# Kernel optimization log

Hardware: AMD Instinct MI355X
Metric: run time of the kernel (lower is better)

The kernel has to match this reference:

```python
import jax, jax.numpy as jnp
import numpy as np

N, C_IN, C_OUT, W, K = 4, 64, 64, 81920, 10


def setup_inputs() -> dict:
    key = jax.random.key(0)
    k1, k2, k3, k4 = jax.random.split(key, 4)
    inp = {}
    inp["input"] = jax.random.normal(k1, (N, C_IN, 1, W), dtype=jnp.float32)
    inp["conv_table"] = jax.random.randint(k2, (W, K), 0, W, dtype=jnp.int64)
    # kaiming-uniform-like init for weight, uniform for bias (values are arbitrary for a numeric baseline)
    fan_in = C_IN * K  # in_dim * 10 * 1
    wb = float(np.sqrt(6.0 / fan_in))
    inp["weight"] = jax.random.uniform(k3, (C_OUT, C_IN, K, 1), dtype=jnp.float32, minval=-wb, maxval=wb)
    bb = float(1.0 / np.sqrt(fan_in))
    inp["bias"] = jax.random.uniform(k4, (C_OUT,), dtype=jnp.float32, minval=-bb, maxval=bb)
    return inp


def reference(input, conv_table, weight, bias):
    # input: (N, C, 1, W); conv_table: (W, 10) neighbor indices into W.
    # Torch: x = input[..., conv_table.T].squeeze() -> (N, C, 10, W); conv2d with (O, C, 10, 1)
    # kernel collapses the neighbor axis: a fixed-adjacency gather + per-pixel weighted sum.
    x = input[:, :, 0, :]                  # (N, C, W)
    gathered = x[:, :, conv_table]         # (N, C, W, 10)  -- irregular gather
    out = jnp.einsum("ncwk,ock->now", gathered, weight[..., 0])  # (N, O, W)
    out = out + bias[None, :, None]
    out = jax.nn.relu(out)
    return out[:, :, None, :]              # (N, O, 1, W) to match conv2d output
```

## Files before the change

### kernel.cpp

```cpp
#include <hip/hip_runtime.h>
#include <hip/hip_bf16.h>

#define N_    4
#define W_    81920
#define K_    10
#define CIO   64

typedef unsigned short u16;
typedef __attribute__((ext_vector_type(8))) short bf16x8;
typedef __attribute__((ext_vector_type(4))) float f32x4;

static __device__ __forceinline__ u16 f2bf(float f) {
    union { float f; unsigned u; } v; v.f = f;
    unsigned r = (v.u + 0x7FFFu + ((v.u >> 16) & 1u)) >> 16;
    return (u16)r;
}

__global__ __launch_bounds__(256) void prep_weights_k(const float* __restrict__ w,
                                                      u16* __restrict__ wfrag) {
    int g = blockIdx.x * 256 + threadIdx.x;
    if (g >= 5120) return;
    int lane = g & 63;
    int f = g >> 6;
    int ot = f & 3, s = f >> 2;
    int o  = ot * 16 + (lane & 15);
    int kb = s * 32 + (lane >> 4) * 8;
    bf16x8 pack;
#pragma unroll
    for (int j = 0; j < 8; ++j) {
        int kappa = kb + j;
        int kt = kappa >> 6, c = kappa & 63;
        pack[j] = (short)f2bf(w[((size_t)o * 64 + c) * K_ + kt]);
    }
    ((bf16x8*)wfrag)[g] = pack;
}

__global__ __launch_bounds__(256) void transpose_k(const float* __restrict__ x,
                                                   unsigned* __restrict__ xTu) {
    __shared__ float tile[64][65];
    int b  = blockIdx.x;
    int n  = b / (W_ / 64), wt = b % (W_ / 64);
    int w0 = wt * 64;
    int tid = threadIdx.x;
    int tx = tid & 63, ty = tid >> 6;
    const float* xn = x + (size_t)n * 64 * W_;
#pragma unroll
    for (int i = 0; i < 16; ++i) {
        int c = ty + 4 * i;
        tile[c][tx] = xn[(size_t)c * W_ + w0 + tx];
    }
    __syncthreads();
    int cx = tid & 31, wy = tid >> 5;
#pragma unroll
    for (int i = 0; i < 8; ++i) {
        int wloc = wy + 8 * i;
        u16 u0 = f2bf(tile[2 * cx][wloc]);
        u16 u1 = f2bf(tile[2 * cx + 1][wloc]);
        xTu[((size_t)n * W_ + w0 + wloc) * 32 + cx] = (unsigned)u0 | ((unsigned)u1 << 16);
    }
}

__global__ __launch_bounds__(512, 2)
void conv_main_k(const u16* __restrict__ xT, const bf16x8* __restrict__ wfrag,
                 const int* __restrict__ table, const float* __restrict__ bias,
                 float* __restrict__ out) {
    __shared__ bf16x8 ldsW[5120];
    __shared__ int    ldsIdx[2560];
    __shared__ float  ldsBias[64];

    const int tid  = threadIdx.x;
    const int lane = tid & 63;
    const int wave = tid >> 6;
    const int b    = blockIdx.x;
    const int n    = b / 320;
    const int w0   = (b % 320) * 256;

    {
        const f32x4* src = (const f32x4*)wfrag;
        f32x4* dst = (f32x4*)ldsW;
#pragma unroll
        for (int i = 0; i < 10; ++i) dst[i * 512 + tid] = src[i * 512 + tid];
    }
    {
        const int* t = table + (size_t)w0 * K_;
        for (int i = tid; i < 2560; i += 512) {
            int wl = i / K_, k = i - wl * K_;
            ldsIdx[k * 256 + wl] = t[i] << 7;
        }
    }
    if (tid < 64) ldsBias[tid] = bias[tid];
    __syncthreads();

    const int quad = lane >> 4;
    const int l15  = lane & 15;
    const int qb   = quad * 16;
    const char* xTn = (const char*)(xT + (size_t)n * W_ * 64);
    const int wbase = wave * 32;

    f32x4 acc[4][2];
#pragma unroll
    for (int ot = 0; ot < 4; ++ot)
#pragma unroll
        for (int mt = 0; mt < 2; ++mt)
#pragma unroll
            for (int r = 0; r < 4; ++r) acc[ot][mt][r] = 0.f;

    auto loadB = [&](int s, int mt) -> bf16x8 {
        int off = ldsIdx[(s >> 1) * 256 + wbase + mt * 16 + l15];
        return *(const bf16x8*)(xTn + off + ((s & 1) * 64 + qb));
    };

    bf16x8 bbuf[4][2];
#pragma unroll
    for (int p = 0; p < 4; ++p) {
        bbuf[p][0] = loadB(p, 0);
        bbuf[p][1] = loadB(p, 1);
    }

#pragma unroll
    for (int s = 0; s < 20; ++s) {
        bf16x8 b0 = bbuf[s & 3][0];
        bf16x8 b1 = bbuf[s & 3][1];
        if (s + 4 < 20) {
            bbuf[s & 3][0] = loadB(s + 4, 0);
            bbuf[s & 3][1] = loadB(s + 4, 1);
        }
#pragma unroll
        for (int ot = 0; ot < 4; ++ot) {
            bf16x8 a = ldsW[(s * 4 + ot) * 64 + lane];
            acc[ot][0] = __builtin_amdgcn_mfma_f32_16x16x32_bf16(a, b0, acc[ot][0], 0, 0, 0);
            acc[ot][1] = __builtin_amdgcn_mfma_f32_16x16x32_bf16(a, b1, acc[ot][1], 0, 0, 0);
        }
    }

#pragma unroll
    for (int ot = 0; ot < 4; ++ot)
#pragma unroll
        for (int mt = 0; mt < 2; ++mt) {
            int wg = w0 + wbase + mt * 16 + l15;
#pragma unroll
            for (int r = 0; r < 4; ++r) {
                int o = ot * 16 + quad * 4 + r;
                float v = acc[ot][mt][r] + ldsBias[o];
                v = v > 0.f ? v : 0.f;
                out[(size_t)(n * 64 + o) * W_ + wg] = v;
            }
        }
}

__global__ __launch_bounds__(256) void naive_k(const float* __restrict__ x,
                                               const int* __restrict__ tb,
                                               const float* __restrict__ wt,
                                               const float* __restrict__ bias,
                                               float* __restrict__ out) {
    size_t g = (size_t)blockIdx.x * 256 + threadIdx.x;
    if (g >= (size_t)N_ * 64 * W_) return;
    int w = (int)(g % W_);
    size_t t = g / W_;
    int o = (int)(t % 64);
    int n = (int)(t / 64);
    float s = bias[o];
    for (int k = 0; k < K_; ++k) {
        int idx = tb[(size_t)w * K_ + k];
        for (int c = 0; c < 64; ++c)
            s += x[((size_t)n * 64 + c) * W_ + idx] * wt[((size_t)o * 64 + c) * K_ + k];
    }
    out[g] = s > 0.f ? s : 0.f;
}

extern "C" void kernel_launch(void* const* d_in, const int* in_sizes, int n_in,
                              void* d_out, int out_size, void* d_ws, size_t ws_size,
                              hipStream_t stream) {
    const float* input  = (const float*)d_in[0];
    const int*   table  = (const int*)d_in[1];
    const float* weight = (const float*)d_in[2];
    const float* bias   = (const float*)d_in[3];
    float* out = (float*)d_out;

    const size_t xT_bytes = (size_t)N_ * W_ * 64 * 2;
    const size_t need     = xT_bytes + 5120 * 16;

    if (ws_size < need) {
        size_t total = (size_t)N_ * 64 * W_;
        naive_k<<<(int)((total + 255) / 256), 256, 0, stream>>>(input, table, weight, bias, out);
        return;
    }

    u16* xT    = (u16*)d_ws;
    u16* wfrag = (u16*)((char*)d_ws + xT_bytes);

    prep_weights_k<<<20, 256, 0, stream>>>(weight, wfrag);
    transpose_k<<<N_ * (W_ / 64), 256, 0, stream>>>(input, (unsigned*)xT);
    conv_main_k<<<1280, 512, 0, stream>>>(xT, (const bf16x8*)wfrag, table, bias, out);
}
```

Baseline: 226.3 us.

## Vectorize transpose and output stores, keep gather indices in registers, swap MFMA operands

The transpose kernel now handles 256 columns per block, reading with float4 loads and writing 8-byte packed bf16 stores. The main kernel loads neighbor indices straight into registers instead of staging them through LDS, and reads bias from global memory. It also swaps the MFMA A/B operands so each lane's accumulator covers 4 consecutive output pixels, which allows 16-byte vector stores of the result. Launch bounds rise to 4 blocks per SM to raise occupancy, at the cost of register pressure from the per-thread offset arrays.

```diff
diff --git a/kernel.cpp b/kernel.cpp
--- a/kernel.cpp
+++ b/kernel.cpp
@@ -4,7 +4,6 @@
 #define N_    4
 #define W_    81920
 #define K_    10
-#define CIO   64
 
 typedef unsigned short u16;
 typedef __attribute__((ext_vector_type(8))) short bf16x8;
@@ -36,37 +35,48 @@
 }
 
 __global__ __launch_bounds__(256) void transpose_k(const float* __restrict__ x,
-                                                   unsigned* __restrict__ xTu) {
+                                                   uint2* __restrict__ xTu) {
     __shared__ float tile[64][65];
     int b  = blockIdx.x;
-    int n  = b / (W_ / 64), wt = b % (W_ / 64);
-    int w0 = wt * 64;
-    int tid = threadIdx.x;
-    int tx = tid & 63, ty = tid >> 6;
+    int n  = b / 320, wt = b % 320;
+    int w0 = wt * 256;
+    int t  = threadIdx.x;
+    int k15 = t & 15, r4 = t >> 4;
     const float* xn = x + (size_t)n * 64 * W_;
 #pragma unroll
-    for (int i = 0; i < 16; ++i) {
-        int c = ty + 4 * i;
-        tile[c][tx] = xn[(size_t)c * W_ + w0 + tx];
-    }
-    __syncthreads();
-    int cx = tid & 31, wy = tid >> 5;
-#pragma unroll
-    for (int i = 0; i < 8; ++i) {
-        int wloc = wy + 8 * i;
-        u16 u0 = f2bf(tile[2 * cx][wloc]);
-        u16 u1 = f2bf(tile[2 * cx + 1][wloc]);
-        xTu[((size_t)n * W_ + w0 + wloc) * 32 + cx] = (unsigned)u0 | ((unsigned)u1 << 16);
-    }
-}
-
-__global__ __launch_bounds__(512, 2)
+    for (int st = 0; st < 4; ++st) {
+        int wst = w0 + st * 64;
+#pragma unroll
+        for (int p = 0; p < 4; ++p) {
+            int c = r4 + 16 * p;
+            float4 v = *(const float4*)&xn[(size_t)c * W_ + wst + k15 * 4];
+            tile[c][k15 * 4 + 0] = v.x;
+            tile[c][k15 * 4 + 1] = v.y;
+            tile[c][k15 * 4 + 2] = v.z;
+            tile[c][k15 * 4 + 3] = v.w;
+        }
+        __syncthreads();
+#pragma unroll
+        for (int q = 0; q < 4; ++q) {
+            int w = r4 + 16 * q;
+            u16 b0 = f2bf(tile[k15 * 4 + 0][w]);
+            u16 b1 = f2bf(tile[k15 * 4 + 1][w]);
+            u16 b2 = f2bf(tile[k15 * 4 + 2][w]);
+            u16 b3 = f2bf(tile[k15 * 4 + 3][w]);
+            uint2 val;
+            val.x = (unsigned)b0 | ((unsigned)b1 << 16);
+            val.y = (unsigned)b2 | ((unsigned)b3 << 16);
+            xTu[(size_t)(n * W_ + wst + w) * 16 + k15] = val;
+        }
+        if (st < 3) __syncthreads();
+    }
+}
+
+__global__ __launch_bounds__(512, 4)
 void conv_main_k(const u16* __restrict__ xT, const bf16x8* __restrict__ wfrag,
                  const int* __restrict__ table, const float* __restrict__ bias,
                  float* __restrict__ out) {
     __shared__ bf16x8 ldsW[5120];
-    __shared__ int    ldsIdx[2560];
-    __shared__ float  ldsBias[64];
 
     const int tid  = threadIdx.x;
     const int lane = tid & 63;
@@ -74,6 +84,8 @@
     const int b    = blockIdx.x;
     const int n    = b / 320;
     const int w0   = (b % 320) * 256;
+    const int quad = lane >> 4;
+    const int l15  = lane & 15;
 
     {
         const f32x4* src = (const f32x4*)wfrag;
@@ -81,21 +93,28 @@
 #pragma unroll
         for (int i = 0; i < 10; ++i) dst[i * 512 + tid] = src[i * 512 + tid];
     }
+
+    const int wbase = wave * 32;
+    int offA[10], offB[10];
     {
-        const int* t = table + (size_t)w0 * K_;
-        for (int i = tid; i < 2560; i += 512) {
-            int wl = i / K_, k = i - wl * K_;
-            ldsIdx[k * 256 + wl] = t[i] << 7;
-        }
-    }
-    if (tid < 64) ldsBias[tid] = bias[tid];
-    __syncthreads();
-
-    const int quad = lane >> 4;
-    const int l15  = lane & 15;
-    const int qb   = quad * 16;
+        const int2* p0 = (const int2*)(table + (size_t)(w0 + wbase + l15) * K_);
+        const int2* p1 = (const int2*)(table + (size_t)(w0 + wbase + 16 + l15) * K_);
+#pragma unroll
+        for (int j = 0; j < 5; ++j) {
+            int2 a = p0[j], c = p1[j];
+            offA[2 * j]     = a.x << 7;
+            offA[2 * j + 1] = a.y << 7;
+            offB[2 * j]     = c.x << 7;
+            offB[2 * j + 1] = c.y << 7;
+        }
+    }
+
+    float bv[4];
+#pragma unroll
+    for (int ot = 0; ot < 4; ++ot) bv[ot] = bias[ot * 16 + l15];
+
     const char* xTn = (const char*)(xT + (size_t)n * W_ * 64);
-    const int wbase = wave * 32;
+    const int qoff = quad * 16;
 
     f32x4 acc[4][2];
 #pragma unroll
@@ -106,8 +125,8 @@
             for (int r = 0; r < 4; ++r) acc[ot][mt][r] = 0.f;
 
     auto loadB = [&](int s, int mt) -> bf16x8 {
-        int off = ldsIdx[(s >> 1) * 256 + wbase + mt * 16 + l15];
-        return *(const bf16x8*)(xTn + off + ((s & 1) * 64 + qb));
+        int off = (mt ? offB : offA)[s >> 1];
+        return *(const bf16x8*)(xTn + (size_t)off + ((s & 1) * 64 + qoff));
     };
 
     bf16x8 bbuf[4][2];
@@ -116,36 +135,39 @@
         bbuf[p][0] = loadB(p, 0);
         bbuf[p][1] = loadB(p, 1);
     }
+    __syncthreads();
 
 #pragma unroll
     for (int s = 0; s < 20; ++s) {
-        bf16x8 b0 = bbuf[s & 3][0];
-        bf16x8 b1 = bbuf[s & 3][1];
+        bf16x8 g0 = bbuf[s & 3][0];
+        bf16x8 g1 = bbuf[s & 3][1];
         if (s + 4 < 20) {
             bbuf[s & 3][0] = loadB(s + 4, 0);
             bbuf[s & 3][1] = loadB(s + 4, 1);
         }
 #pragma unroll
         for (int ot = 0; ot < 4; ++ot) {
-            bf16x8 a = ldsW[(s * 4 + ot) * 64 + lane];
-            acc[ot][0] = __builtin_amdgcn_mfma_f32_16x16x32_bf16(a, b0, acc[ot][0], 0, 0, 0);
-            acc[ot][1] = __builtin_amdgcn_mfma_f32_16x16x32_bf16(a, b1, acc[ot][1], 0, 0, 0);
-        }
-    }
-
-#pragma unroll
-    for (int ot = 0; ot < 4; ++ot)
+            bf16x8 wf = ldsW[(s * 4 + ot) * 64 + lane];
+            acc[ot][0] = __builtin_amdgcn_mfma_f32_16x16x32_bf16(g0, wf, acc[ot][0], 0, 0, 0);
+            acc[ot][1] = __builtin_amdgcn_mfma_f32_16x16x32_bf16(g1, wf, acc[ot][1], 0, 0, 0);
+        }
+    }
+
+#pragma unroll
+    for (int ot = 0; ot < 4; ++ot) {
+        int o = ot * 16 + l15;
 #pragma unroll
         for (int mt = 0; mt < 2; ++mt) {
-            int wg = w0 + wbase + mt * 16 + l15;
+            int wq = w0 + wbase + mt * 16 + quad * 4;
+            f32x4 v = acc[ot][mt];
 #pragma unroll
             for (int r = 0; r < 4; ++r) {
-                int o = ot * 16 + quad * 4 + r;
-                float v = acc[ot][mt][r] + ldsBias[o];
-                v = v > 0.f ? v : 0.f;
-                out[(size_t)(n * 64 + o) * W_ + wg] = v;
+                float f = v[r] + bv[ot];
+                v[r] = f > 0.f ? f : 0.f;
             }
-        }
+            *(f32x4*)&out[(size_t)(n * 64 + o) * W_ + wq] = v;
+        }
+    }
 }
 
 __global__ __launch_bounds__(256) void naive_k(const float* __restrict__ x,
@@ -190,6 +212,6 @@
     u16* wfrag = (u16*)((char*)d_ws + xT_bytes);
 
     prep_weights_k<<<20, 256, 0, stream>>>(weight, wfrag);
-    transpose_k<<<N_ * (W_ / 64), 256, 0, stream>>>(input, (unsigned*)xT);
+    transpose_k<<<N_ * (W_ / 256), 256, 0, stream>>>(input, (uint2*)xT);
     conv_main_k<<<1280, 512, 0, stream>>>(xT, (const bf16x8*)wfrag, table, bias, out);
 }
```

Result: no change. 224.5 us (-0.8%).
